# Optimization experiments

Measured on AMD Instinct MI355X. Metric: run time of the kernel, lower is better.

The kernel has to match this reference:

```python
import jax, jax.numpy as jnp
import numpy as np

HEADS = 4
HID = 610
KER = 50  # cov2KerSize
NEG_SLOPE = 0.2


def gat_layer(x, src, dst, w, b, att_src, att_dst, n_nodes):
    # x: [N, Fin], w: [HEADS*HID, Fin], att_*: [1, HEADS, HID], b: [HID]
    h = (x @ w.T).reshape(n_nodes, HEADS, HID)               # [N,H,D]
    a_src = (h * att_src).sum(-1)                            # [N,H]
    a_dst = (h * att_dst).sum(-1)                            # [N,H]
    alpha = jax.nn.leaky_relu(a_src[src] + a_dst[dst], NEG_SLOPE)  # [E,H]
    # softmax over edges grouped by destination node
    m = jax.ops.segment_max(alpha, dst, num_segments=n_nodes)
    e = jnp.exp(alpha - m[dst])
    denom = jax.ops.segment_sum(e, dst, num_segments=n_nodes)
    a = e / (denom[dst] + 1e-16)                             # [E,H]
    msg = h[src] * a[:, :, None]                             # [E,H,D]
    out = jax.ops.segment_sum(msg, dst, num_segments=n_nodes)  # [N,H,D]
    return out.mean(axis=1) + b                              # [N,D] (concat=False)


def setup_inputs() -> dict:
    key = jax.random.key(0)
    ks = jax.random.split(key, 16)
    N, E, FIN, NOUT = 20000, 100000, 128, 86
    x = jax.random.normal(ks[0], (N, FIN), dtype=jnp.float32)
    edge_index = jax.random.randint(ks[1], (2, E), 0, N, dtype=jnp.int64)
    def kaiming(k, shape, fan_in):
        return jax.random.normal(k, shape, dtype=jnp.float32) * np.float32(np.sqrt(2.0 / fan_in))
    w0 = kaiming(ks[2], (HEADS * HID, FIN), FIN)
    b0 = jnp.zeros((HID,), jnp.float32)
    att_src0 = kaiming(ks[3], (1, HEADS, HID), HID)
    att_dst0 = kaiming(ks[4], (1, HEADS, HID), HID)
    w2 = kaiming(ks[5], (HEADS * HID, HID), HID)
    b2 = jnp.zeros((HID,), jnp.float32)
    att_src1 = kaiming(ks[6], (1, HEADS, HID), HID)
    att_dst1 = kaiming(ks[7], (1, HEADS, HID), HID)
    w4 = kaiming(ks[8], (1, 1, 2, KER), 2 * KER)
    b4 = jnp.zeros((1,), jnp.float32)
    w6 = kaiming(ks[9], (1, 1, KER), KER)
    b6 = jnp.zeros((1,), jnp.float32)
    w8 = kaiming(ks[10], (NOUT, 512), 512)
    b8 = jnp.zeros((NOUT,), jnp.float32)
    return dict(x=x, edge_index=edge_index, w0=w0, b0=b0, att_src0=att_src0,
                att_dst0=att_dst0, w2=w2, b2=b2, att_src1=att_src1,
                att_dst1=att_dst1, w4=w4, b4=b4, w6=w6, b6=b6, w8=w8, b8=b8)


def reference(x, edge_index, w0, b0, att_src0, att_dst0, w2, b2, att_src1,
              att_dst1, w4, b4, w6, b6, w8, b8):
    N = x.shape[0]
    src, dst = edge_index[0], edge_index[1]
    x1 = jax.nn.relu(gat_layer(x, src, dst, w0, b0, att_src0, att_dst0, N))
    x2 = jax.nn.relu(gat_layer(x1, src, dst, w2, b2, att_src1, att_dst1, N))
    # edge features: cat(src_feat, dst_feat) viewed as [E,1,2,HID]
    ef = jnp.stack([x2[src], x2[dst]], axis=1)[:, None, :, :]  # [E,1,2,HID]
    y = jax.lax.conv_general_dilated(ef, w4, (1, 1), 'VALID',
                                     dimension_numbers=('NCHW', 'OIHW', 'NCHW'))
    y = jax.nn.relu(y + b4[None, :, None, None])               # [E,1,1,561]
    y = y.reshape(-1, HID - KER + 1, 1).transpose(0, 2, 1)     # [E,1,561]
    y = jax.lax.conv_general_dilated(y, w6, (1,), 'VALID',
                                     dimension_numbers=('NCH', 'OIH', 'NCH'))
    y = jax.nn.relu(y + b6[None, :, None])                     # [E,1,512]
    # adaptive_avg_pool1d to 512 is identity since length is already 512
    y = y.reshape(-1, 512)
    return y @ w8.T + b8                                       # [E, num_outputs]
```

## Files before the change

kernel.cpp:

```cpp
#include <hip/hip_runtime.h>
#include <math.h>

#define HEADS 4
#define HID 610
#define HIDP 640
#define FIN 128
#define KER 50
#define NOUT 86
#define NEG_SLOPE 0.2f

typedef short bf8_t __attribute__((ext_vector_type(8)));
typedef float f4_t __attribute__((ext_vector_type(4)));

__device__ __forceinline__ ushort f2bf(float f) {
    unsigned u = __float_as_uint(f);
    unsigned r = (u + 0x7FFFu + ((u >> 16) & 1u)) >> 16;
    return (ushort)r;
}
__device__ __forceinline__ float bf2f(ushort b) { return __uint_as_float(((unsigned)b) << 16); }

__global__ void fill_val(float* __restrict__ p, float v, long n) {
    long i = (long)blockIdx.x * blockDim.x + threadIdx.x;
    if (i < n) p[i] = v;
}

__global__ void copy_int(const int* __restrict__ a, int* __restrict__ b, int n) {
    int i = blockIdx.x * blockDim.x + threadIdx.x;
    if (i < n) b[i] = a[i];
}

__global__ void hist_k(const int* __restrict__ ei, int* __restrict__ hist, int E) {
    int e = blockIdx.x * blockDim.x + threadIdx.x;
    if (e < E) atomicAdd(&hist[ei[E + e]], 1);
}

__global__ __launch_bounds__(1024) void scan_k(const int* __restrict__ hist,
                                               int* __restrict__ base, int Nn) {
    __shared__ int tmp[1024];
    __shared__ int carry;
    if (threadIdx.x == 0) carry = 0;
    __syncthreads();
    for (int c0 = 0; c0 < Nn; c0 += 1024) {
        int i = c0 + threadIdx.x;
        int v = (i < Nn) ? hist[i] : 0;
        tmp[threadIdx.x] = v;
        __syncthreads();
        for (int off = 1; off < 1024; off <<= 1) {
            int t = (threadIdx.x >= off) ? tmp[threadIdx.x - off] : 0;
            __syncthreads();
            tmp[threadIdx.x] += t;
            __syncthreads();
        }
        if (i < Nn) base[i] = carry + tmp[threadIdx.x] - v;
        __syncthreads();
        if (threadIdx.x == 1023) carry += tmp[1023];
        __syncthreads();
    }
    if (threadIdx.x == 0) base[Nn] = carry;
}

__global__ void scatter_k(const int* __restrict__ ei, int* __restrict__ cursor,
                          int* __restrict__ esrc, int E) {
    int e = blockIdx.x * blockDim.x + threadIdx.x;
    if (e >= E) return;
    int d = ei[E + e];
    int pos = atomicAdd(&cursor[d], 1);
    esrc[pos] = ei[e];
}

__global__ void split_pad(const float* __restrict__ in, ushort* __restrict__ hi,
                          ushort* __restrict__ lo, int R, int K, int Kp) {
    long i = (long)blockIdx.x * blockDim.x + threadIdx.x;
    if (i >= (long)R * Kp) return;
    int r = (int)(i / Kp), c = (int)(i % Kp);
    float v = (c < K) ? in[(long)r * K + c] : 0.f;
    ushort h = f2bf(v);
    hi[i] = h;
    lo[i] = f2bf(v - bf2f(h));
}

template <int AMODE, bool BIAS>
__global__ __launch_bounds__(256) void gemm_mfma(const float* __restrict__ A,
                                                 const ushort* __restrict__ Aghi,
                                                 const ushort* __restrict__ Aglo,
                                                 const ushort* __restrict__ Bghi,
                                                 const ushort* __restrict__ Bglo,
                                                 const float* __restrict__ bias,
                                                 float* __restrict__ C,
                                                 int M, int N, int Kp) {
    __shared__ __align__(16) ushort Ah[128 * 32];
    __shared__ __align__(16) ushort Al[128 * 32];
    __shared__ __align__(16) ushort Bh[128 * 32];
    __shared__ __align__(16) ushort Bl[128 * 32];
    int tid = threadIdx.x;
    int wave = tid >> 6, lane = tid & 63;
    int quad = lane >> 4, l16 = lane & 15;
    int wm = wave & 1, wn = wave >> 1;
    int row0 = blockIdx.y * 128, col0 = blockIdx.x * 128;

    float4 pa0[4];
    uint4 pah[2], pal[2], pbh[2], pbl[2];

    auto loadA = [&](int k0) {
        if (AMODE == 0) {
#pragma unroll
            for (int q = 0; q < 4; q++) {
                int p = tid + q * 256;
                int r = p >> 3, c4 = (p & 7) << 2;
                int gr = row0 + r;
                pa0[q] = (gr < M) ? *(const float4*)(A + (size_t)gr * Kp + k0 + c4)
                                  : make_float4(0.f, 0.f, 0.f, 0.f);
            }
        } else {
#pragma unroll
            for (int q = 0; q < 2; q++) {
                int p = tid + q * 256;
                int r = p >> 2, c = p & 3;
                int gr = row0 + r;
                if (gr < M) {
                    pah[q] = *(const uint4*)(Aghi + (size_t)gr * Kp + k0 + c * 8);
                    pal[q] = *(const uint4*)(Aglo + (size_t)gr * Kp + k0 + c * 8);
                } else {
                    pah[q] = make_uint4(0, 0, 0, 0);
                    pal[q] = make_uint4(0, 0, 0, 0);
                }
            }
        }
    };
    auto loadB = [&](int k0) {
#pragma unroll
        for (int q = 0; q < 2; q++) {
            int p = tid + q * 256;
            int r = p >> 2, c = p & 3;
            int gr = col0 + r;
            if (gr < N) {
                pbh[q] = *(const uint4*)(Bghi + (size_t)gr * Kp + k0 + c * 8);
                pbl[q] = *(const uint4*)(Bglo + (size_t)gr * Kp + k0 + c * 8);
            } else {
                pbh[q] = make_uint4(0, 0, 0, 0);
                pbl[q] = make_uint4(0, 0, 0, 0);
            }
        }
    };
    auto writeLDS = [&]() {
        if (AMODE == 0) {
#pragma unroll
            for (int q = 0; q < 4; q++) {
                int p = tid + q * 256;
                int r = p >> 3, m = p & 7;
                int pos = r * 32 + ((((m >> 1)) ^ ((r >> 1) & 3)) << 3) + ((m & 1) << 2);
                float4 v = pa0[q];
                ushort4 hv, lv;
                hv.x = f2bf(v.x); lv.x = f2bf(v.x - bf2f(hv.x));
                hv.y = f2bf(v.y); lv.y = f2bf(v.y - bf2f(hv.y));
                hv.z = f2bf(v.z); lv.z = f2bf(v.z - bf2f(hv.z));
                hv.w = f2bf(v.w); lv.w = f2bf(v.w - bf2f(hv.w));
                *(ushort4*)&Ah[pos] = hv;
                *(ushort4*)&Al[pos] = lv;
            }
        } else {
#pragma unroll
            for (int q = 0; q < 2; q++) {
                int p = tid + q * 256;
                int r = p >> 2, c = p & 3;
                int pos = r * 32 + ((c ^ ((r >> 1) & 3)) << 3);
                *(uint4*)&Ah[pos] = pah[q];
                *(uint4*)&Al[pos] = pal[q];
            }
        }
#pragma unroll
        for (int q = 0; q < 2; q++) {
            int p = tid + q * 256;
            int r = p >> 2, c = p & 3;
            int pos = r * 32 + ((c ^ ((r >> 1) & 3)) << 3);
            *(uint4*)&Bh[pos] = pbh[q];
            *(uint4*)&Bl[pos] = pbl[q];
        }
    };

    f4_t acc[4][4];
#pragma unroll
    for (int i = 0; i < 4; i++)
#pragma unroll
        for (int j = 0; j < 4; j++) acc[i][j] = (f4_t){0.f, 0.f, 0.f, 0.f};

    loadA(0);
    loadB(0);
    int sw = (quad ^ ((l16 >> 1) & 3)) << 3;
    for (int k0 = 0; k0 < Kp; k0 += 32) {
        __syncthreads();
        writeLDS();
        __syncthreads();
        if (k0 + 32 < Kp) {
            loadA(k0 + 32);
            loadB(k0 + 32);
        }
        bf8_t ah[4], al[4], bh[4], bl[4];
#pragma unroll
        for (int t = 0; t < 4; t++) {
            int ar = wm * 64 + t * 16 + l16;
            ah[t] = *(const bf8_t*)&Ah[ar * 32 + sw];
            al[t] = *(const bf8_t*)&Al[ar * 32 + sw];
            int br = wn * 64 + t * 16 + l16;
            bh[t] = *(const bf8_t*)&Bh[br * 32 + sw];
            bl[t] = *(const bf8_t*)&Bl[br * 32 + sw];
        }
#pragma unroll
        for (int i = 0; i < 4; i++)
#pragma unroll
            for (int j = 0; j < 4; j++) {
                acc[i][j] = __builtin_amdgcn_mfma_f32_16x16x32_bf16(ah[i], bh[j], acc[i][j], 0, 0, 0);
                acc[i][j] = __builtin_amdgcn_mfma_f32_16x16x32_bf16(al[i], bh[j], acc[i][j], 0, 0, 0);
                acc[i][j] = __builtin_amdgcn_mfma_f32_16x16x32_bf16(ah[i], bl[j], acc[i][j], 0, 0, 0);
            }
    }
#pragma unroll
    for (int i = 0; i < 4; i++) {
#pragma unroll
        for (int r = 0; r < 4; r++) {
            int grow = row0 + wm * 64 + i * 16 + quad * 4 + r;
            if (grow >= M) continue;
#pragma unroll
            for (int j = 0; j < 4; j++) {
                int gcol = col0 + wn * 64 + j * 16 + l16;
                if (gcol >= N) continue;
                float v = acc[i][j][r];
                if (BIAS) v += bias[gcol];
                C[(size_t)grow * N + gcol] = v;
            }
        }
    }
}

__global__ __launch_bounds__(256) void attn_dots(const float* __restrict__ h,
                                                 const float* __restrict__ att_s,
                                                 const float* __restrict__ att_d,
                                                 float* __restrict__ a_src,
                                                 float* __restrict__ a_dst, int Nn) {
    int n = blockIdx.x;
    int head = threadIdx.x >> 6;
    int lane = threadIdx.x & 63;
    const float2* hr = (const float2*)(h + (long)n * (HEADS * HID) + head * HID);
    const float2* as = (const float2*)(att_s + head * HID);
    const float2* ad = (const float2*)(att_d + head * HID);
    float ss = 0.f, sd = 0.f;
    for (int d = lane; d < HID / 2; d += 64) {
        float2 hv = hr[d], av = as[d], dv = ad[d];
        ss += hv.x * av.x + hv.y * av.y;
        sd += hv.x * dv.x + hv.y * dv.y;
    }
    for (int off = 32; off > 0; off >>= 1) {
        ss += __shfl_down(ss, off);
        sd += __shfl_down(sd, off);
    }
    if (lane == 0) {
        a_src[n * HEADS + head] = ss;
        a_dst[n * HEADS + head] = sd;
    }
}

template <int OUTMODE>
__global__ __launch_bounds__(256) void node_aggregate(
    const float* __restrict__ h, const float* __restrict__ asrc,
    const float* __restrict__ adst, const int* __restrict__ base,
    const int* __restrict__ esrc, const float* __restrict__ bias,
    float* __restrict__ xout, ushort* __restrict__ xhi, ushort* __restrict__ xlo,
    int Nn) {
    int wave = threadIdx.x >> 6, lane = threadIdx.x & 63;
    int n = blockIdx.x * 4 + wave;
    if (n >= Nn) return;
    int b0 = base[n], deg = base[n + 1] - b0;
    float ad[HEADS];
#pragma unroll
    for (int hh = 0; hh < HEADS; hh++) ad[hh] = adst[n * HEADS + hh];
    float m[HEADS] = {-INFINITY, -INFINITY, -INFINITY, -INFINITY};
    for (int eb = 0; eb < deg; eb += 64) {
        int i = eb + lane;
        if (i < deg) {
            int s = esrc[b0 + i];
#pragma unroll
            for (int hh = 0; hh < HEADS; hh++) {
                float v = asrc[s * HEADS + hh] + ad[hh];
                v = v >= 0.f ? v : NEG_SLOPE * v;
                m[hh] = fmaxf(m[hh], v);
            }
        }
    }
#pragma unroll
    for (int off = 32; off > 0; off >>= 1)
#pragma unroll
        for (int hh = 0; hh < HEADS; hh++) m[hh] = fmaxf(m[hh], __shfl_xor(m[hh], off));
    float sden[HEADS] = {0.f, 0.f, 0.f, 0.f};
    for (int eb = 0; eb < deg; eb += 64) {
        int i = eb + lane;
        if (i < deg) {
            int s = esrc[b0 + i];
#pragma unroll
            for (int hh = 0; hh < HEADS; hh++) {
                float v = asrc[s * HEADS + hh] + ad[hh];
                v = v >= 0.f ? v : NEG_SLOPE * v;
                sden[hh] += expf(v - m[hh]);
            }
        }
    }
#pragma unroll
    for (int off = 32; off > 0; off >>= 1)
#pragma unroll
        for (int hh = 0; hh < HEADS; hh++) sden[hh] += __shfl_xor(sden[hh], off);
    float inv[HEADS];
#pragma unroll
    for (int hh = 0; hh < HEADS; hh++) inv[hh] = 0.25f / (sden[hh] + 1e-16f);
    float acc0[10] = {}, acc1[10] = {}, acc2[10] = {}, acc3[10] = {};
    for (int eb = 0; eb < deg; eb += 64) {
        int i = eb + lane;
        int sreg = 0;
        float coef[HEADS] = {0.f, 0.f, 0.f, 0.f};
        if (i < deg) {
            sreg = esrc[b0 + i];
#pragma unroll
            for (int hh = 0; hh < HEADS; hh++) {
                float v = asrc[sreg * HEADS + hh] + ad[hh];
                v = v >= 0.f ? v : NEG_SLOPE * v;
                coef[hh] = expf(v - m[hh]) * inv[hh];
            }
        }
        int cnt = deg - eb < 64 ? deg - eb : 64;
        for (int j = 0; j < cnt; j++) {
            int s = __shfl(sreg, j);
            float c0 = __shfl(coef[0], j), c1 = __shfl(coef[1], j);
            float c2 = __shfl(coef[2], j), c3 = __shfl(coef[3], j);
            const float* hr = h + (size_t)s * (HEADS * HID);
#pragma unroll
            for (int t = 0; t < 10; t++) {
                int d = lane + t * 64;
                if (d < HID) {
                    acc0[t] = fmaf(c0, hr[d], acc0[t]);
                    acc1[t] = fmaf(c1, hr[HID + d], acc1[t]);
                    acc2[t] = fmaf(c2, hr[2 * HID + d], acc2[t]);
                    acc3[t] = fmaf(c3, hr[3 * HID + d], acc3[t]);
                }
            }
        }
    }
#pragma unroll
    for (int t = 0; t < 10; t++) {
        int d = lane + t * 64;
        if (d < HID) {
            float v = acc0[t] + acc1[t] + acc2[t] + acc3[t] + bias[d];
            v = v > 0.f ? v : 0.f;
            if (OUTMODE == 0) {
                xout[(size_t)n * HIDP + d] = v;
            } else {
                ushort hv = f2bf(v);
                xhi[(size_t)n * HIDP + d] = hv;
                xlo[(size_t)n * HIDP + d] = f2bf(v - bf2f(hv));
            }
        }
    }
    for (int d = HID + lane; d < HIDP; d += 64) {
        if (OUTMODE == 0) {
            xout[(size_t)n * HIDP + d] = 0.f;
        } else {
            xhi[(size_t)n * HIDP + d] = 0;
            xlo[(size_t)n * HIDP + d] = 0;
        }
    }
}

__device__ __forceinline__ int ystag(int j) { return j + (j >> 3); }

__global__ __launch_bounds__(256) void edge_conv(const float* __restrict__ x2,
                                                 const int* __restrict__ ei,
                                                 const float* __restrict__ w4,
                                                 const float* __restrict__ b4,
                                                 const float* __restrict__ w6,
                                                 const float* __restrict__ b6,
                                                 ushort* __restrict__ zhi,
                                                 ushort* __restrict__ zlo, int E) {
    __shared__ __align__(16) float2 st[4][632];
    __shared__ __align__(16) float y[4][652];
    int wave = threadIdx.x >> 6;
    int lane = threadIdx.x & 63;
    int e = blockIdx.x * 4 + wave;
    bool active = (e < E);
    if (active) {
        int sidx = ei[e];
        int didx = ei[E + e];
        const float2* sp = (const float2*)(x2 + (long)sidx * HIDP);
        const float2* tp = (const float2*)(x2 + (long)didx * HIDP);
        for (int i = lane; i < HID / 2; i += 64) {
            float2 sv = sp[i], tv = tp[i];
            *(float4*)&st[wave][2 * i] = make_float4(sv.x, tv.x, sv.y, tv.y);
        }
    }
    __syncthreads();
    float bb4 = b4[0], bb6 = b6[0];
    if (active) {
        int j0 = lane * 9;
        float acc[9];
        float2 W[18];
#pragma unroll
        for (int i = 0; i < 9; i++) acc[i] = bb4;
#pragma unroll
        for (int p = 0; p < 18; p++) W[p] = st[wave][j0 + p];
#pragma unroll
        for (int g = 0; g < 6; g++) {
#pragma unroll
            for (int mm = 0; mm < 9; mm++) {
                int k = 9 * g + mm;
                if (k < KER) {
                    float ws_ = w4[k], wt_ = w4[KER + k];
#pragma unroll
                    for (int i = 0; i < 9; i++) {
                        float2 v = W[(9 * g + mm + i) % 18];
                        acc[i] = fmaf(v.x, ws_, acc[i]);
                        acc[i] = fmaf(v.y, wt_, acc[i]);
                    }
                }
            }
            if (g < 5) {
#pragma unroll
                for (int p = 0; p < 9; p++)
                    W[(9 * g + p) % 18] = st[wave][j0 + 9 * g + 18 + p];
            }
        }
#pragma unroll
        for (int i = 0; i < 9; i++)
            y[wave][ystag(j0 + i)] = acc[i] > 0.f ? acc[i] : 0.f;
    }
    __syncthreads();
    if (active) {
        int j0 = lane * 8;
        float acc[8];
        float Y[16];
#pragma unroll
        for (int i = 0; i < 8; i++) acc[i] = bb6;
#pragma unroll
        for (int p = 0; p < 16; p++) Y[p] = y[wave][ystag(j0 + p)];
#pragma unroll
        for (int g = 0; g < 7; g++) {
#pragma unroll
            for (int mm = 0; mm < 8; mm++) {
                int k = 8 * g + mm;
                if (k < KER) {
                    float wv = w6[k];
#pragma unroll
                    for (int i = 0; i < 8; i++)
                        acc[i] = fmaf(Y[(8 * g + mm + i) % 16], wv, acc[i]);
                }
            }
            if (g < 6) {
#pragma unroll
                for (int p = 0; p < 8; p++)
                    Y[(8 * g + p) % 16] = y[wave][ystag(j0 + 8 * g + 16 + p)];
            }
        }
        ushort4 zh0, zh1, zl0, zl1;
        float v;
        v = acc[0] > 0.f ? acc[0] : 0.f; zh0.x = f2bf(v); zl0.x = f2bf(v - bf2f(zh0.x));
        v = acc[1] > 0.f ? acc[1] : 0.f; zh0.y = f2bf(v); zl0.y = f2bf(v - bf2f(zh0.y));
        v = acc[2] > 0.f ? acc[2] : 0.f; zh0.z = f2bf(v); zl0.z = f2bf(v - bf2f(zh0.z));
        v = acc[3] > 0.f ? acc[3] : 0.f; zh0.w = f2bf(v); zl0.w = f2bf(v - bf2f(zh0.w));
        v = acc[4] > 0.f ? acc[4] : 0.f; zh1.x = f2bf(v); zl1.x = f2bf(v - bf2f(zh1.x));
        v = acc[5] > 0.f ? acc[5] : 0.f; zh1.y = f2bf(v); zl1.y = f2bf(v - bf2f(zh1.y));
        v = acc[6] > 0.f ? acc[6] : 0.f; zh1.z = f2bf(v); zl1.z = f2bf(v - bf2f(zh1.z));
        v = acc[7] > 0.f ? acc[7] : 0.f; zh1.w = f2bf(v); zl1.w = f2bf(v - bf2f(zh1.w));
        size_t zo = (size_t)e * 512 + j0;
        *(ushort4*)&zhi[zo] = zh0;
        *(ushort4*)&zhi[zo + 4] = zh1;
        *(ushort4*)&zlo[zo] = zl0;
        *(ushort4*)&zlo[zo + 4] = zl1;
    }
}

extern "C" void kernel_launch(void* const* d_in, const int* in_sizes, int n_in,
                              void* d_out, int out_size, void* d_ws, size_t ws_size,
                              hipStream_t stream) {
    const float* x = (const float*)d_in[0];
    const int* ei = (const int*)d_in[1];
    const float* w0 = (const float*)d_in[2];
    const float* b0 = (const float*)d_in[3];
    const float* att_s0 = (const float*)d_in[4];
    const float* att_d0 = (const float*)d_in[5];
    const float* w2 = (const float*)d_in[6];
    const float* b2 = (const float*)d_in[7];
    const float* att_s1 = (const float*)d_in[8];
    const float* att_d1 = (const float*)d_in[9];
    const float* w4 = (const float*)d_in[10];
    const float* b4 = (const float*)d_in[11];
    const float* w6 = (const float*)d_in[12];
    const float* b6 = (const float*)d_in[13];
    const float* w8 = (const float*)d_in[14];
    const float* b8 = (const float*)d_in[15];
    float* out = (float*)d_out;

    const int Nn = in_sizes[0] / FIN;
    const int E = in_sizes[1] / 2;
    const int HD = HEADS * HID;

    float* ws = (float*)d_ws;
    size_t o = 0;
    float* buf1 = ws + o; o += (size_t)Nn * HIDP;
    ushort* x1hi = (ushort*)buf1;
    ushort* x1lo = x1hi + (size_t)Nn * HIDP;
    ushort* w8hi = (ushort*)(ws + o);
    ushort* w8lo = w8hi + (size_t)NOUT * 512; o += (size_t)NOUT * 512;
    ushort* zhi = (ushort*)(ws + o);
    ushort* zlo = zhi + (size_t)E * 512;
    int* base = (int*)(ws + o); o += (size_t)Nn + 4;
    int* cursor = (int*)(ws + o); o += (size_t)Nn;
    int* esrc = (int*)(ws + o); o += (size_t)E;
    float* asrc = ws + o; o += (size_t)Nn * HEADS;
    float* adst = ws + o; o += (size_t)Nn * HEADS;
    ushort* w0hi = (ushort*)(ws + o);
    ushort* w0lo = w0hi + (size_t)HD * FIN; o += (size_t)HD * FIN;
    ushort* w2hi = (ushort*)(ws + o);
    ushort* w2lo = w2hi + (size_t)HD * HIDP; o += (size_t)HD * HIDP;
    float* h = ws + o;

    int edgeGrid = (E + 255) / 256;
    int nodeWaveGrid = (Nn + 3) / 4;
    int edgeConvGrid = (E + 3) / 4;
    dim3 gGemmL((HD + 127) / 128, (Nn + 127) / 128);
    dim3 gGemmF((NOUT + 127) / 128, (E + 127) / 128);

    split_pad<<<((HD * FIN) + 255) / 256, 256, 0, stream>>>(w0, w0hi, w0lo, HD, FIN, FIN);
    split_pad<<<((HD * HIDP) + 255) / 256, 256, 0, stream>>>(w2, w2hi, w2lo, HD, HID, HIDP);
    split_pad<<<((NOUT * 512) + 255) / 256, 256, 0, stream>>>(w8, w8hi, w8lo, NOUT, 512, 512);
    fill_val<<<(Nn + 255) / 256, 256, 0, stream>>>((float*)cursor, 0.f, Nn);
    hist_k<<<edgeGrid, 256, 0, stream>>>(ei, cursor, E);
    scan_k<<<1, 1024, 0, stream>>>(cursor, base, Nn);
    copy_int<<<(Nn + 255) / 256, 256, 0, stream>>>(base, cursor, Nn);
    scatter_k<<<edgeGrid, 256, 0, stream>>>(ei, cursor, esrc, E);

    gemm_mfma<0, false><<<gGemmL, 256, 0, stream>>>(x, nullptr, nullptr, w0hi, w0lo, nullptr,
                                                    h, Nn, HD, FIN);
    attn_dots<<<Nn, 256, 0, stream>>>(h, att_s0, att_d0, asrc, adst, Nn);
    node_aggregate<1><<<nodeWaveGrid, 256, 0, stream>>>(h, asrc, adst, base, esrc, b0,
                                                        nullptr, x1hi, x1lo, Nn);

    gemm_mfma<1, false><<<gGemmL, 256, 0, stream>>>(nullptr, x1hi, x1lo, w2hi, w2lo, nullptr,
                                                    h, Nn, HD, HIDP);
    attn_dots<<<Nn, 256, 0, stream>>>(h, att_s1, att_d1, asrc, adst, Nn);
    node_aggregate<0><<<nodeWaveGrid, 256, 0, stream>>>(h, asrc, adst, base, esrc, b2,
                                                        buf1, nullptr, nullptr, Nn);

    edge_conv<<<edgeConvGrid, 256, 0, stream>>>(buf1, ei, w4, b4, w6, b6, zhi, zlo, E);

    gemm_mfma<1, true><<<gGemmF, 256, 0, stream>>>(nullptr, zhi, zlo, w8hi, w8lo, b8,
                                                   out, E, NOUT, 512);
}
```

Measured before the change: 1.126 ms.

## Fuse edge convolutions and final linear into one MFMA kernel via Toeplitz weights

The two 1D convolutions are recast as matrix multiplies against Toeplitz-expanded weight tiles built once on device. The final projection is fused into the same per-edge kernel, so the large intermediate z buffer (E×512 hi/lo) no longer goes through global memory. Layer-2 node features are now stored as split bf16 hi/lo, which reduces the gather bandwidth per edge. In exchange, the convolutions use split-bf16 MFMA with truncation for the hi part, which adds some precision risk, and the Toeplitz table reuses the w0hi workspace after the first GEMM.

```diff
diff --git a/kernel.cpp b/kernel.cpp
--- a/kernel.cpp
+++ b/kernel.cpp
@@ -9,6 +9,9 @@
 #define NOUT 86
 #define NEG_SLOPE 0.2f
 
+#define Y1S 616
+#define ZSS 520
+
 typedef short bf8_t __attribute__((ext_vector_type(8)));
 typedef float f4_t __attribute__((ext_vector_type(4)));
 
@@ -16,6 +19,9 @@
     unsigned u = __float_as_uint(f);
     unsigned r = (u + 0x7FFFu + ((u >> 16) & 1u)) >> 16;
     return (ushort)r;
+}
+__device__ __forceinline__ ushort f2bf_t(float f) {
+    return (ushort)(__float_as_uint(f) >> 16);
 }
 __device__ __forceinline__ float bf2f(ushort b) { return __uint_as_float(((unsigned)b) << 16); }
 
@@ -77,6 +83,34 @@
     ushort h = f2bf(v);
     hi[i] = h;
     lo[i] = f2bf(v - bf2f(h));
+}
+
+__global__ void build_toeplitz(const float* __restrict__ w4, const float* __restrict__ w6,
+                               ushort* __restrict__ T) {
+    int i = blockIdx.x * blockDim.x + threadIdx.x;
+    if (i >= 18 * 512) return;
+    int e = i & 7;
+    int lane = (i >> 3) & 63;
+    int f = i >> 9;
+    int n = lane & 15;
+    int k = ((lane >> 4) << 3) + e;
+    float wv;
+    int hilo;
+    if (f < 12) {
+        int c = f % 3, hc = f / 3;
+        int ch = hc & 1;
+        hilo = hc >> 1;
+        int d = c * 32 + k - n;
+        wv = (d >= 0 && d < KER) ? w4[ch * KER + d] : 0.f;
+    } else {
+        int r2 = f - 12;
+        int c = r2 % 3;
+        hilo = r2 / 3;
+        int d = c * 32 + k - n;
+        wv = (d >= 0 && d < KER) ? w6[d] : 0.f;
+    }
+    ushort h = f2bf(wv);
+    T[i] = hilo ? f2bf(wv - bf2f(h)) : h;
 }
 
 template <int AMODE, bool BIAS>
@@ -367,109 +401,161 @@
     }
 }
 
-__device__ __forceinline__ int ystag(int j) { return j + (j >> 3); }
-
-__global__ __launch_bounds__(256) void edge_conv(const float* __restrict__ x2,
-                                                 const int* __restrict__ ei,
-                                                 const float* __restrict__ w4,
-                                                 const float* __restrict__ b4,
-                                                 const float* __restrict__ w6,
-                                                 const float* __restrict__ b6,
-                                                 ushort* __restrict__ zhi,
-                                                 ushort* __restrict__ zlo, int E) {
-    __shared__ __align__(16) float2 st[4][632];
-    __shared__ __align__(16) float y[4][652];
-    int wave = threadIdx.x >> 6;
-    int lane = threadIdx.x & 63;
-    int e = blockIdx.x * 4 + wave;
-    bool active = (e < E);
-    if (active) {
-        int sidx = ei[e];
-        int didx = ei[E + e];
-        const float2* sp = (const float2*)(x2 + (long)sidx * HIDP);
-        const float2* tp = (const float2*)(x2 + (long)didx * HIDP);
-        for (int i = lane; i < HID / 2; i += 64) {
-            float2 sv = sp[i], tv = tp[i];
-            *(float4*)&st[wave][2 * i] = make_float4(sv.x, tv.x, sv.y, tv.y);
-        }
+__global__ __launch_bounds__(256, 2) void edge_fused(
+    const ushort* __restrict__ x2hi, const ushort* __restrict__ x2lo,
+    const int* __restrict__ ei, const ushort* __restrict__ T,
+    const float* __restrict__ b4, const float* __restrict__ b6,
+    const ushort* __restrict__ w8hi, const ushort* __restrict__ w8lo,
+    const float* __restrict__ b8, float* __restrict__ out, int E) {
+    __shared__ __align__(16) ushort y1h[32 * Y1S];
+    __shared__ __align__(16) ushort y1l[32 * Y1S];
+    const int tid = threadIdx.x;
+    const int wave = tid >> 6, lane = tid & 63;
+    const int quad = lane >> 4, l16 = lane & 15;
+    const int e0 = blockIdx.x * 32;
+    const int et = wave & 1;
+    const int jb0 = wave >> 1;
+
+    for (int i = tid; i < 32 * (Y1S - 576); i += 256) {
+        int r = i / (Y1S - 576);
+        int j = 576 + (i - r * (Y1S - 576));
+        y1h[r * Y1S + j] = 0;
+        y1l[r * Y1S + j] = 0;
+    }
+
+    bf8_t B1h[2][3], B1l[2][3];
+#pragma unroll
+    for (int ch = 0; ch < 2; ch++)
+#pragma unroll
+        for (int c = 0; c < 3; c++) {
+            B1h[ch][c] = *(const bf8_t*)&T[(ch * 3 + c) * 512 + lane * 8];
+            B1l[ch][c] = *(const bf8_t*)&T[((2 + ch) * 3 + c) * 512 + lane * 8];
+        }
+
+    int eidx = e0 + et * 16 + l16;
+    if (eidx >= E) eidx = E - 1;
+    const ushort* psh = x2hi + (size_t)ei[eidx] * HIDP + quad * 8;
+    const ushort* psl = x2lo + (size_t)ei[eidx] * HIDP + quad * 8;
+    const ushort* pth = x2hi + (size_t)ei[E + eidx] * HIDP + quad * 8;
+    const ushort* ptl = x2lo + (size_t)ei[E + eidx] * HIDP + quad * 8;
+    const float bb4 = b4[0], bb6 = b6[0];
+
+    bf8_t pre0[12], pre1[12];
+    auto ldA = [&](bf8_t(&dst)[12], int jb) {
+        const int o_ = jb * 16;
+#pragma unroll
+        for (int c = 0; c < 3; c++) {
+            dst[c * 4 + 0] = *(const bf8_t*)(psh + o_ + c * 32);
+            dst[c * 4 + 1] = *(const bf8_t*)(psl + o_ + c * 32);
+            dst[c * 4 + 2] = *(const bf8_t*)(pth + o_ + c * 32);
+            dst[c * 4 + 3] = *(const bf8_t*)(ptl + o_ + c * 32);
+        }
+    };
+    auto conv1_tile = [&](const bf8_t(&A)[12], int jb) {
+        const int j0 = jb * 16;
+        f4_t acc = {bb4, bb4, bb4, bb4};
+#pragma unroll
+        for (int c = 0; c < 3; c++) {
+            acc = __builtin_amdgcn_mfma_f32_16x16x32_bf16(A[c * 4 + 0], B1h[0][c], acc, 0, 0, 0);
+            acc = __builtin_amdgcn_mfma_f32_16x16x32_bf16(A[c * 4 + 1], B1h[0][c], acc, 0, 0, 0);
+            acc = __builtin_amdgcn_mfma_f32_16x16x32_bf16(A[c * 4 + 0], B1l[0][c], acc, 0, 0, 0);
+            acc = __builtin_amdgcn_mfma_f32_16x16x32_bf16(A[c * 4 + 2], B1h[1][c], acc, 0, 0, 0);
+            acc = __builtin_amdgcn_mfma_f32_16x16x32_bf16(A[c * 4 + 3], B1h[1][c], acc, 0, 0, 0);
+            acc = __builtin_amdgcn_mfma_f32_16x16x32_bf16(A[c * 4 + 2], B1l[1][c], acc, 0, 0, 0);
+        }
+#pragma unroll
+        for (int r = 0; r < 4; r++) {
+            int e_ = et * 16 + quad * 4 + r;
+            int pos = e_ * Y1S + j0 + l16;
+            float v = acc[r];
+            v = v > 0.f ? v : 0.f;
+            ushort hh = f2bf_t(v);
+            y1h[pos] = hh;
+            y1l[pos] = f2bf(v - bf2f(hh));
+        }
+    };
+
+    ldA(pre0, jb0);
+    for (int tt = 0; tt < 9; tt++) {
+        int jbA = jb0 + 4 * tt;
+        ldA(pre1, jbA + 2);
+        conv1_tile(pre0, jbA);
+        if (tt < 8) ldA(pre0, jbA + 4);
+        conv1_tile(pre1, jbA + 2);
     }
     __syncthreads();
-    float bb4 = b4[0], bb6 = b6[0];
-    if (active) {
-        int j0 = lane * 9;
-        float acc[9];
-        float2 W[18];
-#pragma unroll
-        for (int i = 0; i < 9; i++) acc[i] = bb4;
-#pragma unroll
-        for (int p = 0; p < 18; p++) W[p] = st[wave][j0 + p];
-#pragma unroll
-        for (int g = 0; g < 6; g++) {
-#pragma unroll
-            for (int mm = 0; mm < 9; mm++) {
-                int k = 9 * g + mm;
-                if (k < KER) {
-                    float ws_ = w4[k], wt_ = w4[KER + k];
-#pragma unroll
-                    for (int i = 0; i < 9; i++) {
-                        float2 v = W[(9 * g + mm + i) % 18];
-                        acc[i] = fmaf(v.x, ws_, acc[i]);
-                        acc[i] = fmaf(v.y, wt_, acc[i]);
-                    }
-                }
-            }
-            if (g < 5) {
-#pragma unroll
-                for (int p = 0; p < 9; p++)
-                    W[(9 * g + p) % 18] = st[wave][j0 + 9 * g + 18 + p];
-            }
-        }
-#pragma unroll
-        for (int i = 0; i < 9; i++)
-            y[wave][ystag(j0 + i)] = acc[i] > 0.f ? acc[i] : 0.f;
+
+    bf8_t B2h[3], B2l[3];
+#pragma unroll
+    for (int c = 0; c < 3; c++) {
+        B2h[c] = *(const bf8_t*)&T[(12 + c) * 512 + lane * 8];
+        B2l[c] = *(const bf8_t*)&T[(15 + c) * 512 + lane * 8];
+    }
+    const int arow1 = (et * 16 + l16) * Y1S + quad * 8;
+    f4_t zac[16];
+#pragma unroll
+    for (int t = 0; t < 16; t++) {
+        const int j02 = (jb0 + 2 * t) * 16;
+        f4_t acc = {bb6, bb6, bb6, bb6};
+#pragma unroll
+        for (int c = 0; c < 3; c++) {
+            bf8_t ah = *(const bf8_t*)&y1h[arow1 + j02 + c * 32];
+            bf8_t al = *(const bf8_t*)&y1l[arow1 + j02 + c * 32];
+            acc = __builtin_amdgcn_mfma_f32_16x16x32_bf16(ah, B2h[c], acc, 0, 0, 0);
+            acc = __builtin_amdgcn_mfma_f32_16x16x32_bf16(al, B2h[c], acc, 0, 0, 0);
+            acc = __builtin_amdgcn_mfma_f32_16x16x32_bf16(ah, B2l[c], acc, 0, 0, 0);
+        }
+#pragma unroll
+        for (int r = 0; r < 4; r++) {
+            float v = acc[r];
+            zac[t][r] = v > 0.f ? v : 0.f;
+        }
     }
     __syncthreads();
-    if (active) {
-        int j0 = lane * 8;
-        float acc[8];
-        float Y[16];
-#pragma unroll
-        for (int i = 0; i < 8; i++) acc[i] = bb6;
-#pragma unroll
-        for (int p = 0; p < 16; p++) Y[p] = y[wave][ystag(j0 + p)];
-#pragma unroll
-        for (int g = 0; g < 7; g++) {
-#pragma unroll
-            for (int mm = 0; mm < 8; mm++) {
-                int k = 8 * g + mm;
-                if (k < KER) {
-                    float wv = w6[k];
-#pragma unroll
-                    for (int i = 0; i < 8; i++)
-                        acc[i] = fmaf(Y[(8 * g + mm + i) % 16], wv, acc[i]);
-                }
-            }
-            if (g < 6) {
-#pragma unroll
-                for (int p = 0; p < 8; p++)
-                    Y[(8 * g + p) % 16] = y[wave][ystag(j0 + 8 * g + 16 + p)];
-            }
-        }
-        ushort4 zh0, zh1, zl0, zl1;
-        float v;
-        v = acc[0] > 0.f ? acc[0] : 0.f; zh0.x = f2bf(v); zl0.x = f2bf(v - bf2f(zh0.x));
-        v = acc[1] > 0.f ? acc[1] : 0.f; zh0.y = f2bf(v); zl0.y = f2bf(v - bf2f(zh0.y));
-        v = acc[2] > 0.f ? acc[2] : 0.f; zh0.z = f2bf(v); zl0.z = f2bf(v - bf2f(zh0.z));
-        v = acc[3] > 0.f ? acc[3] : 0.f; zh0.w = f2bf(v); zl0.w = f2bf(v - bf2f(zh0.w));
-        v = acc[4] > 0.f ? acc[4] : 0.f; zh1.x = f2bf(v); zl1.x = f2bf(v - bf2f(zh1.x));
-        v = acc[5] > 0.f ? acc[5] : 0.f; zh1.y = f2bf(v); zl1.y = f2bf(v - bf2f(zh1.y));
-        v = acc[6] > 0.f ? acc[6] : 0.f; zh1.z = f2bf(v); zl1.z = f2bf(v - bf2f(zh1.z));
-        v = acc[7] > 0.f ? acc[7] : 0.f; zh1.w = f2bf(v); zl1.w = f2bf(v - bf2f(zh1.w));
-        size_t zo = (size_t)e * 512 + j0;
-        *(ushort4*)&zhi[zo] = zh0;
-        *(ushort4*)&zhi[zo + 4] = zh1;
-        *(ushort4*)&zlo[zo] = zl0;
-        *(ushort4*)&zlo[zo + 4] = zl1;
+
+#pragma unroll
+    for (int t = 0; t < 16; t++) {
+        const int j02 = (jb0 + 2 * t) * 16;
+#pragma unroll
+        for (int r = 0; r < 4; r++) {
+            int e_ = et * 16 + quad * 4 + r;
+            int pos = e_ * ZSS + j02 + l16;
+            float v = zac[t][r];
+            ushort hh = f2bf_t(v);
+            y1h[pos] = hh;
+            y1l[pos] = f2bf(v - bf2f(hh));
+        }
+    }
+    __syncthreads();
+
+#pragma unroll
+    for (int it = 0; it < 3; it++) {
+        const int item = wave + it * 4;
+        const int et2 = item & 1, nt = item >> 1;
+        const int col = nt * 16 + l16;
+        const int wrow = col < NOUT ? col : 0;
+        const float bias = col < NOUT ? b8[col] : 0.f;
+        f4_t acc = {bias, bias, bias, bias};
+        const int arow = (et2 * 16 + l16) * ZSS + quad * 8;
+        const ushort* wph = w8hi + (size_t)wrow * 512 + quad * 8;
+        const ushort* wpl = w8lo + (size_t)wrow * 512 + quad * 8;
+#pragma unroll
+        for (int c = 0; c < 16; c++) {
+            bf8_t zh = *(const bf8_t*)&y1h[arow + c * 32];
+            bf8_t zl = *(const bf8_t*)&y1l[arow + c * 32];
+            bf8_t wh = *(const bf8_t*)(wph + c * 32);
+            bf8_t wl = *(const bf8_t*)(wpl + c * 32);
+            acc = __builtin_amdgcn_mfma_f32_16x16x32_bf16(zh, wh, acc, 0, 0, 0);
+            acc = __builtin_amdgcn_mfma_f32_16x16x32_bf16(zl, wh, acc, 0, 0, 0);
+            acc = __builtin_amdgcn_mfma_f32_16x16x32_bf16(zh, wl, acc, 0, 0, 0);
+        }
+        if (col < NOUT) {
+#pragma unroll
+            for (int r = 0; r < 4; r++) {
+                int e_ = e0 + et2 * 16 + quad * 4 + r;
+                if (e_ < E) out[(size_t)e_ * NOUT + col] = acc[r];
+            }
+        }
     }
 }
 
@@ -505,8 +591,6 @@
     ushort* x1lo = x1hi + (size_t)Nn * HIDP;
     ushort* w8hi = (ushort*)(ws + o);
     ushort* w8lo = w8hi + (size_t)NOUT * 512; o += (size_t)NOUT * 512;
-    ushort* zhi = (ushort*)(ws + o);
-    ushort* zlo = zhi + (size_t)E * 512;
     int* base = (int*)(ws + o); o += (size_t)Nn + 4;
     int* cursor = (int*)(ws + o); o += (size_t)Nn;
     int* esrc = (int*)(ws + o); o += (size_t)E;
@@ -520,9 +604,8 @@
 
     int edgeGrid = (E + 255) / 256;
     int nodeWaveGrid = (Nn + 3) / 4;
-    int edgeConvGrid = (E + 3) / 4;
+    int fusedGrid = (E + 31) / 32;
     dim3 gGemmL((HD + 127) / 128, (Nn + 127) / 128);
-    dim3 gGemmF((NOUT + 127) / 128, (E + 127) / 128);
 
     split_pad<<<((HD * FIN) + 255) / 256, 256, 0, stream>>>(w0, w0hi, w0lo, HD, FIN, FIN);
     split_pad<<<((HD * HIDP) + 255) / 256, 256, 0, stream>>>(w2, w2hi, w2lo, HD, HID, HIDP);
@@ -535,6 +618,7 @@
 
     gemm_mfma<0, false><<<gGemmL, 256, 0, stream>>>(x, nullptr, nullptr, w0hi, w0lo, nullptr,
                                                     h, Nn, HD, FIN);
+    build_toeplitz<<<(18 * 512 + 255) / 256, 256, 0, stream>>>(w4, w6, w0hi);
     attn_dots<<<Nn, 256, 0, stream>>>(h, att_s0, att_d0, asrc, adst, Nn);
     node_aggregate<1><<<nodeWaveGrid, 256, 0, stream>>>(h, asrc, adst, base, esrc, b0,
                                                         nullptr, x1hi, x1lo, Nn);
@@ -542,11 +626,9 @@
     gemm_mfma<1, false><<<gGemmL, 256, 0, stream>>>(nullptr, x1hi, x1lo, w2hi, w2lo, nullptr,
                                                     h, Nn, HD, HIDP);
     attn_dots<<<Nn, 256, 0, stream>>>(h, att_s1, att_d1, asrc, adst, Nn);
-    node_aggregate<0><<<nodeWaveGrid, 256, 0, stream>>>(h, asrc, adst, base, esrc, b2,
-                                                        buf1, nullptr, nullptr, Nn);
-
-    edge_conv<<<edgeConvGrid, 256, 0, stream>>>(buf1, ei, w4, b4, w6, b6, zhi, zlo, E);
-
-    gemm_mfma<1, true><<<gGemmF, 256, 0, stream>>>(nullptr, zhi, zlo, w8hi, w8lo, b8,
-                                                   out, E, NOUT, 512);
-}
+    node_aggregate<1><<<nodeWaveGrid, 256, 0, stream>>>(h, asrc, adst, base, esrc, b2,
+                                                        nullptr, x1hi, x1lo, Nn);
+
+    edge_fused<<<fusedGrid, 256, 0, stream>>>(x1hi, x1lo, ei, w0hi, b4, b6,
+                                              w8hi, w8lo, b8, out, E);
+}
```

Result: slower. 1.282 ms (+13.8%).
